# Kernel tuning notes

Hardware: AMD Instinct MI355X
Metric: run time of the kernel (lower is better)

## Reference

```python
import jax, jax.numpy as jnp
import numpy as np

B, S, D, H = 2, 2048, 1024, 16
DK = D // H  # 64
SQRT_DK = DK ** 0.5
NEG = -1e9


def setup_inputs() -> dict:
    key = jax.random.key(0)
    ks = jax.random.split(key, 7)
    scale = 1.0 / np.sqrt(D)
    return {
        "x": jax.random.normal(ks[0], (B, S, D), jnp.float32),
        "encoder_output": jax.random.normal(ks[1], (B, S, D), jnp.float32),
        "mask": jax.random.randint(ks[2], (B, S), 0, 2, jnp.int32),
        "WQ": jax.random.normal(ks[3], (D, D), jnp.float32) * scale,
        "WK": jax.random.normal(ks[4], (D, D), jnp.float32) * scale,
        "WV": jax.random.normal(ks[5], (D, D), jnp.float32) * scale,
        "WO": jax.random.normal(ks[6], (D, D), jnp.float32) * scale,
    }


def reference(x, encoder_output, mask, WQ, WK, WV, WO):
    b, s, d = x.shape
    # project and split heads: (b, h, s, dk)
    q = (x @ WQ).reshape(b, s, H, DK).transpose(0, 2, 1, 3)
    k = (encoder_output @ WK).reshape(b, s, H, DK).transpose(0, 2, 1, 3)
    v = (encoder_output @ WV).reshape(b, s, H, DK).transpose(0, 2, 1, 3)
    # scores: (b, h, s_q, s_k)
    scores = jnp.einsum('bhqd,bhkd->bhqk', q, k) / SQRT_DK
    # future mask (strict upper triangle) + padding mask broadcast over key dim
    future = jnp.triu(jnp.ones((s, s), jnp.int32), 1)  # (s, s)
    m = mask[:, None, :, None] + future[None, None, :, :]  # (b, 1->h, s_q, s_k)
    scores = jnp.where(m != 0, NEG, scores)
    attn = jax.nn.softmax(scores, axis=-1)
    # context: (b, s, h, dk) -> (b, s, d)
    ctx = jnp.einsum('bhqk,bhkd->bqhd', attn, v).reshape(b, s, d)
    return ctx @ WO
```

## Files before the change

kernel.cpp:

```cpp
#include <hip/hip_runtime.h>
#include <hip/hip_bf16.h>

constexpr int B = 2, S = 2048, D = 1024, H = 16, DK = 64;
constexpr int M = B * S;
constexpr float LOG2E = 1.44269504088896f;
constexpr float NEGBIG = -3.0e38f;
constexpr float QSCALE = 0.125f * LOG2E;

using short8 = __attribute__((ext_vector_type(8))) short;
using short4v = __attribute__((ext_vector_type(4))) short;
using f32x4 = __attribute__((ext_vector_type(4))) float;

#define GLOBAL_AS __attribute__((address_space(1)))
#define LDS_AS __attribute__((address_space(3)))

__device__ __forceinline__ void gll16(const void* g, void* l) {
  __builtin_amdgcn_global_load_lds((const GLOBAL_AS void*)g, (LDS_AS void*)l, 16, 0, 0);
}

__device__ __forceinline__ short f2bf(float f) {
  __hip_bfloat16 h = __float2bfloat16(f);
  short s;
  __builtin_memcpy(&s, &h, 2);
  return s;
}
__device__ __forceinline__ unsigned pack2bf(float a, float b) {
  return (unsigned)(unsigned short)f2bf(a) | ((unsigned)(unsigned short)f2bf(b) << 16);
}

__global__ __launch_bounds__(256) void prep_kernel(const float* __restrict__ x,
                                                   const float* __restrict__ enc,
                                                   const float* __restrict__ W0,
                                                   const float* __restrict__ W1,
                                                   const float* __restrict__ W2,
                                                   const float* __restrict__ W3,
                                                   short* __restrict__ xb,
                                                   short* __restrict__ encb,
                                                   short* __restrict__ Wt) {
  __shared__ float t[64][65];
  const int bx = blockIdx.x;
  if (bx < 8192) {
    const float4* src = (const float4*)((bx & 4096) ? enc : x);
    short4v* dst = (short4v*)((bx & 4096) ? encb : xb);
    const int i = (bx & 4095) * 256 + threadIdx.x;
    const float4 v = src[i];
    short4v o;
    o[0] = f2bf(v.x); o[1] = f2bf(v.y); o[2] = f2bf(v.z); o[3] = f2bf(v.w);
    dst[i] = o;
  } else {
    const int idx = bx - 8192;
    const int z = idx >> 8, rem = idx & 255;
    const float* W = z == 0 ? W0 : z == 1 ? W1 : z == 2 ? W2 : W3;
    short* dstw = Wt + (size_t)z * D * D;
    const int n0 = (rem & 15) * 64, k0 = (rem >> 4) * 64;
    const int lx = threadIdx.x & 63, ly = threadIdx.x >> 6;
    #pragma unroll
    for (int r = 0; r < 64; r += 4)
      t[r + ly][lx] = W[(size_t)(k0 + r + ly) * D + n0 + lx];
    __syncthreads();
    #pragma unroll
    for (int r = 0; r < 64; r += 4)
      dstw[(size_t)(n0 + r + ly) * D + k0 + lx] = f2bf(t[lx][r + ly]);
  }
}

__global__ __launch_bounds__(256) void gemm_qkv_kernel(const short* __restrict__ A0,
                                                       const short* __restrict__ A1,
                                                       const short* __restrict__ Wts,
                                                       short* __restrict__ Cv,
                                                       float* __restrict__ vsum) {
  __shared__ short As[3][4][128][8];
  __shared__ short Bs[3][4][128][8];
  const int z = blockIdx.z;
  const short* __restrict__ A = z ? A1 : A0;
  const short* __restrict__ Bt = Wts + (size_t)z * D * D;
  const float oscale = (z == 0) ? QSCALE : 1.0f;

  const int tid = threadIdx.x;
  const int lane = tid & 63, wid = tid >> 6;
  const int l15 = lane & 15, lg = lane >> 4;
  const int row0 = blockIdx.x * 128, col0 = blockIdx.y * 128;
  const int wm = wid >> 1, wn = wid & 1;
  f32x4 acc[4][4] = {};
  constexpr int NSTEP = D / 32;

  auto stage = [&](int k0, int nb) {
    #pragma unroll
    for (int it = 0; it < 2; ++it) {
      const int c = tid + it * 256;
      const int row = c & 127, kc2 = c >> 7;
      gll16(&A[(size_t)(row0 + row) * D + k0 + kc2 * 8],
            (char*)As + nb * 8192 + (wid * 64 + it * 256) * 16);
      gll16(&Bt[(size_t)(col0 + row) * D + k0 + kc2 * 8],
            (char*)Bs + nb * 8192 + (wid * 64 + it * 256) * 16);
    }
  };

  stage(0, 0);
  stage(32, 1);
  for (int t = 0; t < NSTEP; ++t) {
    if (t < NSTEP - 1) asm volatile("s_waitcnt vmcnt(4)\ns_barrier" ::: "memory");
    else               asm volatile("s_waitcnt vmcnt(0)\ns_barrier" ::: "memory");
    if (t + 2 < NSTEP) stage((t + 2) * 32, (t + 2) % 3);
    const int cur = t % 3;
    short8 af[4], bfr[4];
    #pragma unroll
    for (int m = 0; m < 4; ++m) af[m] = *(const short8*)&As[cur][lg][wm * 64 + m * 16 + l15][0];
    #pragma unroll
    for (int n = 0; n < 4; ++n) bfr[n] = *(const short8*)&Bs[cur][lg][wn * 64 + n * 16 + l15][0];
    #pragma unroll
    for (int m = 0; m < 4; ++m)
      #pragma unroll
      for (int n = 0; n < 4; ++n)
        acc[m][n] = __builtin_amdgcn_mfma_f32_16x16x32_bf16(af[m], bfr[n], acc[m][n], 0, 0, 0);
  }
  #pragma unroll
  for (int m = 0; m < 4; ++m) {
    #pragma unroll
    for (int r = 0; r < 4; ++r) {
      const int row = row0 + wm * 64 + m * 16 + 4 * lg + r;
      #pragma unroll
      for (int n = 0; n < 4; ++n) {
        const int col = col0 + wn * 64 + n * 16 + l15;
        Cv[(size_t)z * M * D + (size_t)row * D + col] = f2bf(acc[m][n][r] * oscale);
      }
    }
  }
  if (z == 2) {
    const int bidx = row0 >> 11;
    #pragma unroll
    for (int n = 0; n < 4; ++n) {
      float s = 0.f;
      #pragma unroll
      for (int m = 0; m < 4; ++m)
        s += acc[m][n][0] + acc[m][n][1] + acc[m][n][2] + acc[m][n][3];
      s += __shfl_xor(s, 16);
      s += __shfl_xor(s, 32);
      if (lg == 0) atomicAdd(&vsum[(size_t)bidx * D + col0 + wn * 64 + n * 16 + l15], s);
    }
  }
}

__global__ __launch_bounds__(256) void gemmO_kernel(const short* __restrict__ A,
                                                    const short* __restrict__ Bt,
                                                    float* __restrict__ C) {
  __shared__ short As[3][4][128][8];
  __shared__ short Bs[3][4][64][8];
  const int tid = threadIdx.x;
  const int lane = tid & 63, wid = tid >> 6;
  const int l15 = lane & 15, lg = lane >> 4;
  const int row0 = blockIdx.x * 128, col0 = blockIdx.y * 64;
  const int wm = wid >> 1, wn = wid & 1;
  f32x4 acc[4][2] = {};
  constexpr int NSTEP = D / 32;

  auto stage = [&](int k0, int nb) {
    #pragma unroll
    for (int it = 0; it < 2; ++it) {
      const int c = tid + it * 256;
      const int row = c & 127, kc2 = c >> 7;
      gll16(&A[(size_t)(row0 + row) * D + k0 + kc2 * 8],
            (char*)As + nb * 8192 + (wid * 64 + it * 256) * 16);
    }
    gll16(&Bt[(size_t)(col0 + lane) * D + k0 + wid * 8],
          (char*)Bs + nb * 4096 + wid * 1024);
  };

  stage(0, 0);
  stage(32, 1);
  for (int t = 0; t < NSTEP; ++t) {
    if (t < NSTEP - 1) asm volatile("s_waitcnt vmcnt(3)\ns_barrier" ::: "memory");
    else               asm volatile("s_waitcnt vmcnt(0)\ns_barrier" ::: "memory");
    if (t + 2 < NSTEP) stage((t + 2) * 32, (t + 2) % 3);
    const int cur = t % 3;
    short8 af[4], bfr[2];
    #pragma unroll
    for (int m = 0; m < 4; ++m) af[m] = *(const short8*)&As[cur][lg][wm * 64 + m * 16 + l15][0];
    #pragma unroll
    for (int n = 0; n < 2; ++n) bfr[n] = *(const short8*)&Bs[cur][lg][wn * 32 + n * 16 + l15][0];
    #pragma unroll
    for (int m = 0; m < 4; ++m)
      #pragma unroll
      for (int n = 0; n < 2; ++n)
        acc[m][n] = __builtin_amdgcn_mfma_f32_16x16x32_bf16(af[m], bfr[n], acc[m][n], 0, 0, 0);
  }
  #pragma unroll
  for (int m = 0; m < 4; ++m)
    #pragma unroll
    for (int r = 0; r < 4; ++r) {
      const int row = row0 + wm * 64 + m * 16 + 4 * lg + r;
      #pragma unroll
      for (int n = 0; n < 2; ++n)
        C[(size_t)row * D + col0 + wn * 32 + n * 16 + l15] = acc[m][n][r];
    }
}

__device__ __forceinline__ int keyof(int c, int i) {
  return ((c >> 1) << 5) + ((i >> 2) << 3) + ((c & 1) << 2) + (i & 3);
}
__device__ __forceinline__ int vt_byte(int kc, int d, int ksb) {
  return kc * 1024 + ((d ^ (kc & 7)) << 4) + ksb * 2;
}

__global__ __launch_bounds__(512, 4) void attn_kernel(const short* __restrict__ Qb,
                                                      const short* __restrict__ Kb,
                                                      const short* __restrict__ Vb,
                                                      const int* __restrict__ maskp,
                                                      const float* __restrict__ vsum,
                                                      short* __restrict__ ctxb) {
  __shared__ char KsBuf[2][16384];
  __shared__ char VtBuf[2][16384];
  const int bid = blockIdx.x;
  const int qt = 15 - (bid >> 5);
  const int bh = bid & 31;
  const int b = bh >> 4, h = bh & 15;
  const int tid = threadIdx.x, lane = tid & 63, wid = tid >> 6;
  const int l15 = lane & 15, lg = lane >> 4;
  const int ql = wid * 16 + l15;

  short8 qf[2];
  {
    const size_t o = (size_t)(b * S + qt * 128 + ql) * D + h * DK;
    qf[0] = *(const short8*)&Qb[o + lg * 8];
    qf[1] = *(const short8*)&Qb[o + 32 + lg * 8];
  }
  float m = NEGBIG, l = 0.f;
  f32x4 cx[4] = {};

  const int kkey = keyof(lg, l15);
  const int vu = tid & 63, dv = tid >> 6;
  const int vh = vu >> 5, vl = vu & 31;
  const int vkc = vl >> 2, vksb = (vl & 3) * 2;

  auto stageK = [&](int jc, int nb) {
    const size_t base = (size_t)(b * S + jc * 128 + kkey) * D + h * DK + wid * 8;
    gll16(&Kb[base], (char*)KsBuf + nb * 16384 + wid * 1024);
    gll16(&Kb[base + (size_t)64 * D], (char*)KsBuf + nb * 16384 + 8192 + wid * 1024);
  };
  auto loadV = [&](int jc, short8& va, short8& vb2) {
    const size_t vb0 = (size_t)(b * S + jc * 128 + 2 * vu) * D + h * DK + dv * 8;
    va = *(const short8*)&Vb[vb0];
    vb2 = *(const short8*)&Vb[vb0 + D];
  };
  auto writeV = [&](int nb, const short8& va, const short8& vb2) {
    char* dst = (char*)VtBuf + nb * 16384 + vh * 8192;
    #pragma unroll
    for (int i = 0; i < 8; ++i) {
      const unsigned w = (unsigned)(unsigned short)va[i] | ((unsigned)(unsigned short)vb2[i] << 16);
      *(unsigned*)(dst + vt_byte(vkc, dv * 8 + i, vksb)) = w;
    }
  };

  auto tile_pair = [&](int nb, bool do1, bool mask0, bool mask1) {
    const char* ks0 = (const char*)KsBuf + nb * 16384;
    const char* ks1 = ks0 + 8192;
    const char* vt0 = (const char*)VtBuf + nb * 16384;
    const char* vt1 = vt0 + 8192;
    f32x4 sa0[4], sa1[4];
    #pragma unroll
    for (int c = 0; c < 4; ++c) {
      const short8 kf0 = *(const short8*)(ks0 + lg * 1024 + c * 256 + l15 * 16);
      const short8 kf1 = *(const short8*)(ks0 + (4 + lg) * 1024 + c * 256 + l15 * 16);
      f32x4 zz = {0.f, 0.f, 0.f, 0.f};
      zz = __builtin_amdgcn_mfma_f32_16x16x32_bf16(kf0, qf[0], zz, 0, 0, 0);
      zz = __builtin_amdgcn_mfma_f32_16x16x32_bf16(kf1, qf[1], zz, 0, 0, 0);
      sa0[c] = zz;
    }
    if (do1) {
      #pragma unroll
      for (int c = 0; c < 4; ++c) {
        const short8 kf0 = *(const short8*)(ks1 + lg * 1024 + c * 256 + l15 * 16);
        const short8 kf1 = *(const short8*)(ks1 + (4 + lg) * 1024 + c * 256 + l15 * 16);
        f32x4 zz = {0.f, 0.f, 0.f, 0.f};
        zz = __builtin_amdgcn_mfma_f32_16x16x32_bf16(kf0, qf[0], zz, 0, 0, 0);
        zz = __builtin_amdgcn_mfma_f32_16x16x32_bf16(kf1, qf[1], zz, 0, 0, 0);
        sa1[c] = zz;
      }
    }
    if (mask0) {
      #pragma unroll
      for (int c = 0; c < 4; ++c)
        #pragma unroll
        for (int r = 0; r < 4; ++r)
          if (((c >> 1) << 5) + (lg << 3) + ((c & 1) << 2) + r > ql) sa0[c][r] = NEGBIG;
    }
    if (do1 && mask1) {
      #pragma unroll
      for (int c = 0; c < 4; ++c)
        #pragma unroll
        for (int r = 0; r < 4; ++r)
          if (64 + ((c >> 1) << 5) + (lg << 3) + ((c & 1) << 2) + r > ql) sa1[c][r] = NEGBIG;
    }
    float pm = sa0[0][0];
    #pragma unroll
    for (int c = 0; c < 4; ++c)
      #pragma unroll
      for (int r = 0; r < 4; ++r) pm = fmaxf(pm, sa0[c][r]);
    if (do1)
      #pragma unroll
      for (int c = 0; c < 4; ++c)
        #pragma unroll
        for (int r = 0; r < 4; ++r) pm = fmaxf(pm, sa1[c][r]);
    pm = fmaxf(pm, __shfl_xor(pm, 16));
    pm = fmaxf(pm, __shfl_xor(pm, 32));
    if (pm > m + 8.f) {
      const float sc = exp2f(m - pm);
      l *= sc;
      #pragma unroll
      for (int dt = 0; dt < 4; ++dt) cx[dt] *= sc;
      m = pm;
    }
    float rs = 0.f;
    #pragma unroll
    for (int c = 0; c < 4; ++c)
      #pragma unroll
      for (int r = 0; r < 4; ++r) {
        const float p = exp2f(sa0[c][r] - m);
        sa0[c][r] = p;
        rs += p;
      }
    if (do1)
      #pragma unroll
      for (int c = 0; c < 4; ++c)
        #pragma unroll
        for (int r = 0; r < 4; ++r) {
          const float p = exp2f(sa1[c][r] - m);
          sa1[c][r] = p;
          rs += p;
        }
    rs += __shfl_xor(rs, 16);
    rs += __shfl_xor(rs, 32);
    l += rs;
    {
      short8 pf[2];
      #pragma unroll
      for (int kk = 0; kk < 2; ++kk)
        #pragma unroll
        for (int jj = 0; jj < 8; ++jj)
          pf[kk][jj] = f2bf(sa0[kk * 2 + (jj >> 2)][jj & 3]);
      #pragma unroll
      for (int kk = 0; kk < 2; ++kk)
        #pragma unroll
        for (int dt = 0; dt < 4; ++dt) {
          const short8 vf = *(const short8*)(vt0 + vt_byte(kk * 4 + lg, dt * 16 + l15, 0));
          cx[dt] = __builtin_amdgcn_mfma_f32_16x16x32_bf16(vf, pf[kk], cx[dt], 0, 0, 0);
        }
    }
    if (do1) {
      short8 pf[2];
      #pragma unroll
      for (int kk = 0; kk < 2; ++kk)
        #pragma unroll
        for (int jj = 0; jj < 8; ++jj)
          pf[kk][jj] = f2bf(sa1[kk * 2 + (jj >> 2)][jj & 3]);
      #pragma unroll
      for (int kk = 0; kk < 2; ++kk)
        #pragma unroll
        for (int dt = 0; dt < 4; ++dt) {
          const short8 vf = *(const short8*)(vt1 + vt_byte(kk * 4 + lg, dt * 16 + l15, 0));
          cx[dt] = __builtin_amdgcn_mfma_f32_16x16x32_bf16(vf, pf[kk], cx[dt], 0, 0, 0);
        }
    }
  };

  {
    short8 va, vb2;
    stageK(0, 0);
    loadV(0, va, vb2);
    writeV(0, va, vb2);
  }
  __syncthreads();
  int cur = 0;
  for (int jc = 0; jc <= qt; ++jc) {
    short8 nva, nvb;
    if (jc < qt) { stageK(jc + 1, cur ^ 1); loadV(jc + 1, nva, nvb); }
    const bool diag = (jc == qt), hi = (wid >= 4);
    tile_pair(cur, !diag || hi, diag && !hi, diag && hi);
    if (jc < qt) writeV(cur ^ 1, nva, nvb);
    __syncthreads();
    cur ^= 1;
  }

  {
    const int qg = qt * 128 + ql;
    const int mq = maskp[b * S + qg];
    const float inv = 1.0f / l;
    constexpr float vscale = 1.0f / S;
    short* orow = &ctxb[(size_t)(b * S + qg) * D + h * DK];
    const float* vmb = &vsum[(size_t)b * D + h * DK];
    #pragma unroll
    for (int dt = 0; dt < 4; ++dt)
      #pragma unroll
      for (int p2 = 0; p2 < 2; ++p2) {
        const int d = dt * 16 + 4 * lg + p2 * 2;
        const float v0 = mq ? vmb[d] * vscale     : cx[dt][p2 * 2] * inv;
        const float v1 = mq ? vmb[d + 1] * vscale : cx[dt][p2 * 2 + 1] * inv;
        *(unsigned*)&orow[d] = pack2bf(v0, v1);
      }
  }
}

extern "C" void kernel_launch(void* const* d_in, const int* in_sizes, int n_in,
                              void* d_out, int out_size, void* d_ws, size_t ws_size,
                              hipStream_t stream) {
  (void)in_sizes; (void)n_in; (void)out_size; (void)ws_size;
  const float* x   = (const float*)d_in[0];
  const float* enc = (const float*)d_in[1];
  const int*   msk = (const int*)d_in[2];
  const float* WQ  = (const float*)d_in[3];
  const float* WK  = (const float*)d_in[4];
  const float* WV  = (const float*)d_in[5];
  const float* WO  = (const float*)d_in[6];
  float* out = (float*)d_out;

  char* ws = (char*)d_ws;
  const size_t MB = 1u << 20;
  short* xb    = (short*)(ws + 0);
  short* encb  = (short*)(ws + 8 * MB);
  short* Qb    = (short*)(ws + 16 * MB);
  short* WQt   = (short*)(ws + 40 * MB);
  float* vsum  = (float*)(ws + 48 * MB);
  short* Kb    = Qb + (size_t)M * D;
  short* Vb    = Kb + (size_t)M * D;
  short* WOt   = WQt + (size_t)3 * D * D;
  short* ctxb  = xb;

  hipMemsetAsync(vsum, 0, (size_t)B * D * sizeof(float), stream);

  prep_kernel<<<dim3(9216), 256, 0, stream>>>(x, enc, WQ, WK, WV, WO, xb, encb, WQt);

  gemm_qkv_kernel<<<dim3(M / 128, D / 128, 3), 256, 0, stream>>>(xb, encb, WQt, Qb, vsum);

  attn_kernel<<<dim3(512), 512, 0, stream>>>(Qb, Kb, Vb, msk, vsum, ctxb);

  gemmO_kernel<<<dim3(M / 128, D / 64), 256, 0, stream>>>(ctxb, WOt, out);
}
```

Baseline: 166.4 us.

## Switch GEMMs to double-buffered BK=64 pipeline and reorder attention tile schedule

Both the QKV and output-projection GEMMs move from a 3-stage BK=32 pipeline with explicit vmcnt waits to a 2-stage BK=64 double buffer that syncs with __syncthreads. This halves the number of barriers per K sweep and doubles the work between them, at the cost of shallower prefetch and more LDS per block. The attention kernel's query-tile order changes so the first 256 blocks process the heaviest tiles (qt 15 down to 8) and the rest process tiles 0 to 7 in ascending order, which alters load balancing across the causal workload.

```diff
diff --git a/kernel.cpp b/kernel.cpp
--- a/kernel.cpp
+++ b/kernel.cpp
@@ -69,8 +69,8 @@
                                                        const short* __restrict__ Wts,
                                                        short* __restrict__ Cv,
                                                        float* __restrict__ vsum) {
-  __shared__ short As[3][4][128][8];
-  __shared__ short Bs[3][4][128][8];
+  __shared__ short As[2][8][128][8];
+  __shared__ short Bs[2][8][128][8];
   const int z = blockIdx.z;
   const short* __restrict__ A = z ? A1 : A0;
   const short* __restrict__ Bt = Wts + (size_t)z * D * D;
@@ -82,37 +82,42 @@
   const int row0 = blockIdx.x * 128, col0 = blockIdx.y * 128;
   const int wm = wid >> 1, wn = wid & 1;
   f32x4 acc[4][4] = {};
-  constexpr int NSTEP = D / 32;
+  constexpr int NSTEP = D / 64;
 
   auto stage = [&](int k0, int nb) {
     #pragma unroll
-    for (int it = 0; it < 2; ++it) {
+    for (int it = 0; it < 4; ++it) {
       const int c = tid + it * 256;
       const int row = c & 127, kc2 = c >> 7;
       gll16(&A[(size_t)(row0 + row) * D + k0 + kc2 * 8],
-            (char*)As + nb * 8192 + (wid * 64 + it * 256) * 16);
+            (char*)As + nb * 16384 + (wid * 64 + it * 256) * 16);
       gll16(&Bt[(size_t)(col0 + row) * D + k0 + kc2 * 8],
-            (char*)Bs + nb * 8192 + (wid * 64 + it * 256) * 16);
+            (char*)Bs + nb * 16384 + (wid * 64 + it * 256) * 16);
     }
   };
 
   stage(0, 0);
-  stage(32, 1);
+  __syncthreads();
+  int cur = 0;
   for (int t = 0; t < NSTEP; ++t) {
-    if (t < NSTEP - 1) asm volatile("s_waitcnt vmcnt(4)\ns_barrier" ::: "memory");
-    else               asm volatile("s_waitcnt vmcnt(0)\ns_barrier" ::: "memory");
-    if (t + 2 < NSTEP) stage((t + 2) * 32, (t + 2) % 3);
-    const int cur = t % 3;
-    short8 af[4], bfr[4];
-    #pragma unroll
-    for (int m = 0; m < 4; ++m) af[m] = *(const short8*)&As[cur][lg][wm * 64 + m * 16 + l15][0];
-    #pragma unroll
-    for (int n = 0; n < 4; ++n) bfr[n] = *(const short8*)&Bs[cur][lg][wn * 64 + n * 16 + l15][0];
-    #pragma unroll
-    for (int m = 0; m < 4; ++m)
+    if (t < NSTEP - 1) stage((t + 1) * 64, cur ^ 1);
+    #pragma unroll
+    for (int ks = 0; ks < 2; ++ks) {
+      short8 af[4], bfr[4];
+      #pragma unroll
+      for (int m = 0; m < 4; ++m)
+        af[m] = *(const short8*)&As[cur][ks * 4 + lg][wm * 64 + m * 16 + l15][0];
       #pragma unroll
       for (int n = 0; n < 4; ++n)
-        acc[m][n] = __builtin_amdgcn_mfma_f32_16x16x32_bf16(af[m], bfr[n], acc[m][n], 0, 0, 0);
+        bfr[n] = *(const short8*)&Bs[cur][ks * 4 + lg][wn * 64 + n * 16 + l15][0];
+      #pragma unroll
+      for (int m = 0; m < 4; ++m)
+        #pragma unroll
+        for (int n = 0; n < 4; ++n)
+          acc[m][n] = __builtin_amdgcn_mfma_f32_16x16x32_bf16(af[m], bfr[n], acc[m][n], 0, 0, 0);
+    }
+    __syncthreads();
+    cur ^= 1;
   }
   #pragma unroll
   for (int m = 0; m < 4; ++m) {
@@ -144,45 +149,55 @@
 __global__ __launch_bounds__(256) void gemmO_kernel(const short* __restrict__ A,
                                                     const short* __restrict__ Bt,
                                                     float* __restrict__ C) {
-  __shared__ short As[3][4][128][8];
-  __shared__ short Bs[3][4][64][8];
+  __shared__ short As[2][8][128][8];
+  __shared__ short Bs[2][8][64][8];
   const int tid = threadIdx.x;
   const int lane = tid & 63, wid = tid >> 6;
   const int l15 = lane & 15, lg = lane >> 4;
   const int row0 = blockIdx.x * 128, col0 = blockIdx.y * 64;
   const int wm = wid >> 1, wn = wid & 1;
   f32x4 acc[4][2] = {};
-  constexpr int NSTEP = D / 32;
+  constexpr int NSTEP = D / 64;
 
   auto stage = [&](int k0, int nb) {
     #pragma unroll
-    for (int it = 0; it < 2; ++it) {
+    for (int it = 0; it < 4; ++it) {
       const int c = tid + it * 256;
       const int row = c & 127, kc2 = c >> 7;
       gll16(&A[(size_t)(row0 + row) * D + k0 + kc2 * 8],
-            (char*)As + nb * 8192 + (wid * 64 + it * 256) * 16);
-    }
-    gll16(&Bt[(size_t)(col0 + lane) * D + k0 + wid * 8],
-          (char*)Bs + nb * 4096 + wid * 1024);
+            (char*)As + nb * 16384 + (wid * 64 + it * 256) * 16);
+    }
+    #pragma unroll
+    for (int it = 0; it < 2; ++it) {
+      const int c = tid + it * 256;
+      const int row = c & 63, kc2 = c >> 6;
+      gll16(&Bt[(size_t)(col0 + row) * D + k0 + kc2 * 8],
+            (char*)Bs + nb * 8192 + (wid * 64 + it * 256) * 16);
+    }
   };
 
   stage(0, 0);
-  stage(32, 1);
+  __syncthreads();
+  int cur = 0;
   for (int t = 0; t < NSTEP; ++t) {
-    if (t < NSTEP - 1) asm volatile("s_waitcnt vmcnt(3)\ns_barrier" ::: "memory");
-    else               asm volatile("s_waitcnt vmcnt(0)\ns_barrier" ::: "memory");
-    if (t + 2 < NSTEP) stage((t + 2) * 32, (t + 2) % 3);
-    const int cur = t % 3;
-    short8 af[4], bfr[2];
-    #pragma unroll
-    for (int m = 0; m < 4; ++m) af[m] = *(const short8*)&As[cur][lg][wm * 64 + m * 16 + l15][0];
-    #pragma unroll
-    for (int n = 0; n < 2; ++n) bfr[n] = *(const short8*)&Bs[cur][lg][wn * 32 + n * 16 + l15][0];
-    #pragma unroll
-    for (int m = 0; m < 4; ++m)
+    if (t < NSTEP - 1) stage((t + 1) * 64, cur ^ 1);
+    #pragma unroll
+    for (int ks = 0; ks < 2; ++ks) {
+      short8 af[4], bfr[2];
+      #pragma unroll
+      for (int m = 0; m < 4; ++m)
+        af[m] = *(const short8*)&As[cur][ks * 4 + lg][wm * 64 + m * 16 + l15][0];
       #pragma unroll
       for (int n = 0; n < 2; ++n)
-        acc[m][n] = __builtin_amdgcn_mfma_f32_16x16x32_bf16(af[m], bfr[n], acc[m][n], 0, 0, 0);
+        bfr[n] = *(const short8*)&Bs[cur][ks * 4 + lg][wn * 32 + n * 16 + l15][0];
+      #pragma unroll
+      for (int m = 0; m < 4; ++m)
+        #pragma unroll
+        for (int n = 0; n < 2; ++n)
+          acc[m][n] = __builtin_amdgcn_mfma_f32_16x16x32_bf16(af[m], bfr[n], acc[m][n], 0, 0, 0);
+    }
+    __syncthreads();
+    cur ^= 1;
   }
   #pragma unroll
   for (int m = 0; m < 4; ++m)
@@ -211,7 +226,7 @@
   __shared__ char KsBuf[2][16384];
   __shared__ char VtBuf[2][16384];
   const int bid = blockIdx.x;
-  const int qt = 15 - (bid >> 5);
+  const int qt = (bid < 256) ? 15 - (bid >> 5) : (bid >> 5) - 8;
   const int bh = bid & 31;
   const int b = bh >> 4, h = bh & 15;
   const int tid = threadIdx.x, lane = tid & 63, wid = tid >> 6;
```

Result: slower. 184.1 us (+10.6%).
